# Kernel optimization log

Measured on AMD Instinct MI355X. Metric: run time of the kernel, lower is better.

The kernel has to match this reference:

```python
import jax, jax.numpy as jnp
import numpy as np

NUM_HEADS = 8

def _ln(x):
    m = x.mean(-1, keepdims=True)
    v = ((x - m) ** 2).mean(-1, keepdims=True)
    return (x - m) / jnp.sqrt(v + 1e-5)

def _encoder_layer(x, qkv_w, out_w, w1, w2, attn_mask=None):
    # standard post-LN transformer encoder layer; returns output and
    # head-averaged attention probabilities (b, t, t)
    b, t, d = x.shape
    dh = d // NUM_HEADS
    qkv = jnp.einsum('btd,cde->cbte', x, qkv_w)          # (3, b, t, d)
    q, k, v = [a.reshape(b, t, NUM_HEADS, dh).transpose(0, 2, 1, 3) for a in qkv]
    scores = jnp.einsum('bhqd,bhkd->bhqk', q, k) / jnp.sqrt(jnp.asarray(dh, x.dtype))
    if attn_mask is not None:
        scores = scores + attn_mask                       # additive -inf/0 mask
    probs = jax.nn.softmax(scores, axis=-1)
    ctx = jnp.einsum('bhqk,bhkd->bhqd', probs, v)
    ctx = ctx.transpose(0, 2, 1, 3).reshape(b, t, d)
    x = _ln(x + ctx @ out_w)
    x = _ln(x + jax.nn.relu(x @ w1) @ w2)
    return x, probs.mean(axis=1)

def _window_ids(wbool):
    # faithful vectorization of generate_local_window_mask_v2's sequential scan:
    # run-length segmentation of the thresholded weights, where a run of
    # length 1 is absorbed into the following run (weights[frame_start] is
    # overwritten). Returns per-frame window id (T,) int32.
    T = wbool.shape[0]
    def step(carry, t):
        cur, start, wid = carry
        wt = wbool[t]
        same = wt == cur
        merge = (~same) & (start + 1 == t)   # length-1 run absorbed
        close = (~same) & (~merge)           # close window, start new one
        cur = jnp.where(same, cur, wt)
        start = jnp.where(close, t, start)
        wid = wid + close.astype(jnp.int32)
        return (cur, start, wid), wid
    _, ids = jax.lax.scan(step, (wbool[0], jnp.int32(0), jnp.int32(0)), jnp.arange(1, T))
    return jnp.concatenate([jnp.zeros((1,), jnp.int32), ids])

def reference(x, v_qkv_w, v_out_w, v_w1, v_w2, l_qkv_w, l_out_w, l_w1, l_w2):
    b, t, d = x.shape
    # 1) vanilla transformer pass
    out_v, aw_v = _encoder_layer(x, v_qkv_w, v_out_w, v_w1, v_w2)
    # attention received per key token, min-max normalized (normalize_tensor)
    w = aw_v.sum(axis=1)                                   # (b, t)
    wmin = w.min(axis=-1, keepdims=True)
    wmax = w.max(axis=-1, keepdims=True)
    w = (w - wmin) / (wmax - wmin + 1e-8)
    # 2) dynamic window mask generation (threshold = 0.5)
    ids = jax.vmap(_window_ids)(w >= 0.5)                  # (b, t)
    same = ids[:, :, None] == ids[:, None, :]
    attn_mask = jnp.where(same, 0.0, -jnp.inf).astype(x.dtype)   # (b, t, t)
    # window_mapping[b, k, j] = 1 if frame j belongs to window k
    # (kept at full t rows; torch truncates to max_window_count, which is
    #  data-dependent; extra rows here are all-zero)
    window_mapping = (jnp.arange(t, dtype=jnp.int32)[None, :, None] == ids[:, None, :]).astype(x.dtype)
    # 3) dynamic-local-window transformer pass with block-diagonal mask
    out_l, aw_l = _encoder_layer(out_v, l_qkv_w, l_out_w, l_w1, l_w2,
                                 attn_mask=attn_mask[:, None])  # broadcast over heads
    aw_l = jnp.where(jnp.isneginf(aw_l), jnp.zeros_like(aw_l), aw_l)
    wl = jax.nn.softmax(aw_l.sum(axis=1), axis=-1)         # (b, t)
    # 4) window-weighted pooling
    word_tokens = jnp.einsum('bwt,btd->bwd', window_mapping, out_l * wl[:, :, None])
    return jnp.concatenate([word_tokens, x], axis=1), window_mapping

def setup_inputs() -> dict:
    B, T, D, FF = 8, 1024, 512, 2048
    key = jax.random.key(0)
    ks = jax.random.split(key, 9)
    s = 0.02
    return {
        'x': jax.random.normal(ks[0], (B, T, D), jnp.float32),
        'v_qkv_w': jax.random.normal(ks[1], (3, D, D), jnp.float32) * s,
        'v_out_w': jax.random.normal(ks[2], (D, D), jnp.float32) * s,
        'v_w1': jax.random.normal(ks[3], (D, FF), jnp.float32) * s,
        'v_w2': jax.random.normal(ks[4], (FF, D), jnp.float32) * s,
        'l_qkv_w': jax.random.normal(ks[5], (3, D, D), jnp.float32) * s,
        'l_out_w': jax.random.normal(ks[6], (D, D), jnp.float32) * s,
        'l_w1': jax.random.normal(ks[7], (D, FF), jnp.float32) * s,
        'l_w2': jax.random.normal(ks[8], (FF, D), jnp.float32) * s,
    }
```

## Files before the change

kernel.cpp:

```cpp
#include <hip/hip_runtime.h>
#include <math.h>

#define Bz 8
#define Tz 1024
#define Dz 512
#define FFz 2048
#define Hz 8
#define DHz 64
#define Mz (Bz * Tz)

typedef __attribute__((ext_vector_type(8))) short short8;
typedef __attribute__((ext_vector_type(4))) float f32x4;

__device__ inline unsigned short f2bf(float f) {
  unsigned u = __builtin_bit_cast(unsigned, f);
  return (unsigned short)((u + 0x7FFFu + ((u >> 16) & 1u)) >> 16);
}
__device__ inline float bf2f(unsigned short h) {
  unsigned u = (unsigned)h << 16;
  return __builtin_bit_cast(float, u);
}

__device__ inline void attn_decode(int g, int& b, int& h, int& qt) {
  const int xcd = g & 7;
  const int j = g >> 3;
  qt = j & 15;
  const int bh = ((j >> 4) << 3) | xcd;
  b = bh >> 3;
  h = bh & 7;
}

__device__ inline int swz(int row, int slotByte) {
  return row * 128 + (slotByte ^ ((row & 7) << 4));
}

struct WDesc { const float* src; unsigned short* dst; unsigned short* dstlo;
               int K; int N; int blk0; };
struct PrepArgs { WDesc d[12]; int nwc; };

__global__ __launch_bounds__(256) void prep_kernel(PrepArgs P,
    const float* __restrict__ x, unsigned short* __restrict__ xbf,
    unsigned short* __restrict__ xlo, float* __restrict__ csz)
{
  const int bid = blockIdx.x;
  const int tid = threadIdx.x;
  if (bid < P.nwc) {
    int i = 0;
    while (i < 11 && bid >= P.d[i + 1].blk0) ++i;
    const WDesc w = P.d[i];
    const int lb = bid - w.blk0;
    const int nbn = w.N / 32;
    const int bn = (lb % nbn) * 32, bk = (lb / nbn) * 32;
    __shared__ float t[32][33];
    const int tx = tid & 31, ty = tid >> 5;
#pragma unroll
    for (int r = 0; r < 32; r += 8)
      t[ty + r][tx] = w.src[(size_t)(bk + ty + r) * w.N + bn + tx];
    __syncthreads();
#pragma unroll
    for (int r = 0; r < 32; r += 8) {
      float v = t[tx][ty + r];
      unsigned short hv = f2bf(v);
      w.dst[(size_t)(bn + ty + r) * w.K + bk + tx] = hv;
      if (w.dstlo)
        w.dstlo[(size_t)(bn + ty + r) * w.K + bk + tx] = f2bf(v - bf2f(hv));
    }
  } else if (bid < P.nwc + 64) {
    int idx = (bid - P.nwc) * 256 + tid;
    csz[idx] = 0.f;
  } else {
    int i = (bid - P.nwc - 64) * 256 + tid;
    float4 v = *reinterpret_cast<const float4*>(&x[(size_t)i * 4]);
    ushort4 o, ol;
    o.x = f2bf(v.x); o.y = f2bf(v.y); o.z = f2bf(v.z); o.w = f2bf(v.w);
    ol.x = f2bf(v.x - bf2f(o.x)); ol.y = f2bf(v.y - bf2f(o.y));
    ol.z = f2bf(v.z - bf2f(o.z)); ol.w = f2bf(v.w - bf2f(o.w));
    *reinterpret_cast<ushort4*>(&xbf[(size_t)i * 4]) = o;
    *reinterpret_cast<ushort4*>(&xlo[(size_t)i * 4]) = ol;
  }
}

__global__ __launch_bounds__(256) void mfma_gemm_kernel(
    const unsigned short* __restrict__ A, const unsigned short* __restrict__ BT,
    void* __restrict__ p1, void* __restrict__ p2, void* __restrict__ p3,
    int K, int N, int mode)
{
  __shared__ unsigned short As[128 * 32];
  __shared__ unsigned short Bs[128 * 32];
  const int tid = threadIdx.x;
  const int lane = tid & 63, wave = tid >> 6;
  const int mr = lane & 15, quad = lane >> 4;
  const int wr = wave >> 1, wc = wave & 1;
  const int m0 = blockIdx.y * 128;
  const int n0 = blockIdx.x * 128;

  f32x4 acc[4][4];
  const f32x4 zero = {0.f, 0.f, 0.f, 0.f};
#pragma unroll
  for (int i = 0; i < 4; ++i)
#pragma unroll
    for (int j = 0; j < 4; ++j) acc[i][j] = zero;

  const int srow = tid >> 2;
  const int sslot = tid & 3;
  const unsigned short* Ag = A + (size_t)(m0 + srow) * K + sslot * 8;
  const unsigned short* Bg = BT + (size_t)(n0 + srow) * K + sslot * 8;
  char* AsB = (char*)As;
  char* BsB = (char*)Bs;

  for (int k0 = 0; k0 < K; k0 += 32) {
    short8 a0 = *reinterpret_cast<const short8*>(Ag + k0);
    short8 a1 = *reinterpret_cast<const short8*>(Ag + (size_t)64 * K + k0);
    short8 b0 = *reinterpret_cast<const short8*>(Bg + k0);
    short8 b1 = *reinterpret_cast<const short8*>(Bg + (size_t)64 * K + k0);
    *reinterpret_cast<short8*>(AsB + srow * 64 + sslot * 16) = a0;
    *reinterpret_cast<short8*>(AsB + (srow + 64) * 64 + sslot * 16) = a1;
    *reinterpret_cast<short8*>(BsB + srow * 64 + sslot * 16) = b0;
    *reinterpret_cast<short8*>(BsB + (srow + 64) * 64 + sslot * 16) = b1;
    __syncthreads();
    short8 af[4], bf[4];
#pragma unroll
    for (int i = 0; i < 4; ++i)
      af[i] = *reinterpret_cast<const short8*>(AsB + (wr * 64 + i * 16 + mr) * 64 + quad * 16);
#pragma unroll
    for (int j = 0; j < 4; ++j)
      bf[j] = *reinterpret_cast<const short8*>(BsB + (wc * 64 + j * 16 + mr) * 64 + quad * 16);
#pragma unroll
    for (int i = 0; i < 4; ++i)
#pragma unroll
      for (int j = 0; j < 4; ++j)
        acc[i][j] = __builtin_amdgcn_mfma_f32_16x16x32_bf16(af[i], bf[j], acc[i][j], 0, 0, 0);
    __syncthreads();
  }

  const int m0w = m0 + wr * 64;
  const int n0w = n0 + wc * 64;
  int emode = mode;
  unsigned short* Cbf = (unsigned short*)p1;
  unsigned short* Vt  = (unsigned short*)p1;
  int ncol = N, coff = 0;
  if (mode == 5) {
    if (n0w < 512)       { emode = 1; Cbf = (unsigned short*)p1; ncol = 512; coff = 0; }
    else if (n0w < 1024) { emode = 1; Cbf = (unsigned short*)p2; ncol = 512; coff = 512; }
    else                 { emode = 4; Vt = (unsigned short*)p3; coff = 1024; }
  }
  if (emode == 4) {
#pragma unroll
    for (int i = 0; i < 4; ++i)
#pragma unroll
      for (int j = 0; j < 4; ++j) {
        const int col = n0w - coff + j * 16 + mr;
        const int row0 = m0w + i * 16 + quad * 4;
        const int bb = row0 >> 10, t0 = row0 & 1023;
        ushort4 pk;
        pk.x = f2bf(acc[i][j][0]); pk.y = f2bf(acc[i][j][1]);
        pk.z = f2bf(acc[i][j][2]); pk.w = f2bf(acc[i][j][3]);
        *reinterpret_cast<ushort4*>(
            &Vt[((size_t)((bb * Hz + (col >> 6)) * DHz + (col & 63))) * Tz + t0]) = pk;
      }
  } else if (emode == 0) {
    float* Cf = (float*)p1;
#pragma unroll
    for (int i = 0; i < 4; ++i)
#pragma unroll
      for (int j = 0; j < 4; ++j) {
        const int col = n0w + j * 16 + mr;
#pragma unroll
        for (int rr = 0; rr < 4; ++rr)
          Cf[(size_t)(m0w + i * 16 + quad * 4 + rr) * N + col] = acc[i][j][rr];
      }
  } else {
    const bool relu = (emode == 2);
#pragma unroll
    for (int i = 0; i < 4; ++i)
#pragma unroll
      for (int j = 0; j < 4; ++j) {
        const int col = n0w - coff + j * 16 + mr;
#pragma unroll
        for (int rr = 0; rr < 4; ++rr) {
          float v = acc[i][j][rr];
          if (relu) v = fmaxf(v, 0.f);
          Cbf[(size_t)(m0w + i * 16 + quad * 4 + rr) * ncol + col] = f2bf(v);
        }
      }
  }
}

__global__ __launch_bounds__(256) void gemm_qk_mfma_kernel(
    const unsigned short* __restrict__ Xh, const unsigned short* __restrict__ Xl,
    const unsigned short* __restrict__ WQh, const unsigned short* __restrict__ WQl,
    const unsigned short* __restrict__ WKh, const unsigned short* __restrict__ WKl,
    unsigned short* __restrict__ Qhi, unsigned short* __restrict__ Qlo,
    unsigned short* __restrict__ Khi, unsigned short* __restrict__ Klo)
{
  __shared__ unsigned short Ash[128 * 32];
  __shared__ unsigned short Asl[128 * 32];
  __shared__ unsigned short Bsh[128 * 32];
  __shared__ unsigned short Bsl[128 * 32];
  const int tid = threadIdx.x;
  const int lane = tid & 63, wave = tid >> 6;
  const int mr = lane & 15, quad = lane >> 4;
  const int wr = wave >> 1, wc = wave & 1;
  const int sel = blockIdx.y >> 6;
  const int m0 = (blockIdx.y & 63) * 128;
  const int n0 = blockIdx.x * 128;
  const unsigned short* Bh = sel ? WKh : WQh;
  const unsigned short* Bl = sel ? WKl : WQl;
  unsigned short* Chi = sel ? Khi : Qhi;
  unsigned short* Clo = sel ? Klo : Qlo;

  f32x4 acc[4][4];
  const f32x4 zero = {0.f, 0.f, 0.f, 0.f};
#pragma unroll
  for (int i = 0; i < 4; ++i)
#pragma unroll
    for (int j = 0; j < 4; ++j) acc[i][j] = zero;

  const int srow = tid >> 2;
  const int sslot = tid & 3;
  const unsigned short* Ahg = Xh + (size_t)(m0 + srow) * Dz + sslot * 8;
  const unsigned short* Alg = Xl + (size_t)(m0 + srow) * Dz + sslot * 8;
  const unsigned short* Bhg = Bh + (size_t)(n0 + srow) * Dz + sslot * 8;
  const unsigned short* Blg = Bl + (size_t)(n0 + srow) * Dz + sslot * 8;
  char* AhB = (char*)Ash; char* AlB = (char*)Asl;
  char* BhB = (char*)Bsh; char* BlB = (char*)Bsl;

  for (int k0 = 0; k0 < Dz; k0 += 32) {
    short8 ah0 = *reinterpret_cast<const short8*>(Ahg + k0);
    short8 ah1 = *reinterpret_cast<const short8*>(Ahg + (size_t)64 * Dz + k0);
    short8 al0 = *reinterpret_cast<const short8*>(Alg + k0);
    short8 al1 = *reinterpret_cast<const short8*>(Alg + (size_t)64 * Dz + k0);
    short8 bh0 = *reinterpret_cast<const short8*>(Bhg + k0);
    short8 bh1 = *reinterpret_cast<const short8*>(Bhg + (size_t)64 * Dz + k0);
    short8 bl0 = *reinterpret_cast<const short8*>(Blg + k0);
    short8 bl1 = *reinterpret_cast<const short8*>(Blg + (size_t)64 * Dz + k0);
    *reinterpret_cast<short8*>(AhB + srow * 64 + sslot * 16) = ah0;
    *reinterpret_cast<short8*>(AhB + (srow + 64) * 64 + sslot * 16) = ah1;
    *reinterpret_cast<short8*>(AlB + srow * 64 + sslot * 16) = al0;
    *reinterpret_cast<short8*>(AlB + (srow + 64) * 64 + sslot * 16) = al1;
    *reinterpret_cast<short8*>(BhB + srow * 64 + sslot * 16) = bh0;
    *reinterpret_cast<short8*>(BhB + (srow + 64) * 64 + sslot * 16) = bh1;
    *reinterpret_cast<short8*>(BlB + srow * 64 + sslot * 16) = bl0;
    *reinterpret_cast<short8*>(BlB + (srow + 64) * 64 + sslot * 16) = bl1;
    __syncthreads();
    short8 ah[4], al[4], bh[4], bl[4];
#pragma unroll
    for (int i = 0; i < 4; ++i) {
      const int ab = (wr * 64 + i * 16 + mr) * 64 + quad * 16;
      ah[i] = *reinterpret_cast<const short8*>(AhB + ab);
      al[i] = *reinterpret_cast<const short8*>(AlB + ab);
    }
#pragma unroll
    for (int j = 0; j < 4; ++j) {
      const int bb = (wc * 64 + j * 16 + mr) * 64 + quad * 16;
      bh[j] = *reinterpret_cast<const short8*>(BhB + bb);
      bl[j] = *reinterpret_cast<const short8*>(BlB + bb);
    }
#pragma unroll
    for (int i = 0; i < 4; ++i)
#pragma unroll
      for (int j = 0; j < 4; ++j) {
        acc[i][j] = __builtin_amdgcn_mfma_f32_16x16x32_bf16(al[i], bh[j], acc[i][j], 0, 0, 0);
        acc[i][j] = __builtin_amdgcn_mfma_f32_16x16x32_bf16(ah[i], bl[j], acc[i][j], 0, 0, 0);
        acc[i][j] = __builtin_amdgcn_mfma_f32_16x16x32_bf16(ah[i], bh[j], acc[i][j], 0, 0, 0);
      }
    __syncthreads();
  }

  const int m0w = m0 + wr * 64;
  const int n0w = n0 + wc * 64;
#pragma unroll
  for (int i = 0; i < 4; ++i)
#pragma unroll
    for (int j = 0; j < 4; ++j) {
      const int col = n0w + j * 16 + mr;
#pragma unroll
      for (int rr = 0; rr < 4; ++rr) {
        const size_t row = (size_t)(m0w + i * 16 + quad * 4 + rr);
        float v = acc[i][j][rr];
        unsigned short hv = f2bf(v);
        Chi[row * Dz + col] = hv;
        Clo[row * Dz + col] = f2bf(v - bf2f(hv));
      }
    }
}

__global__ __launch_bounds__(256) void attn_z_kernel(
    const unsigned short* __restrict__ Qh, const unsigned short* __restrict__ Kh,
    float* __restrict__ invzG)
{
  __shared__ unsigned short Ksh[64 * 64];
  const int tid = threadIdx.x;
  const int lane = tid & 63, wave = tid >> 6;
  const int c = lane & 15, quad = lane >> 4;
  int b, h, qt;
  attn_decode(blockIdx.x, b, h, qt);
  const size_t bT = (size_t)b * Tz;
  const int qrow = qt * 64 + wave * 16;
  const int hoff = h * DHz;

  const size_t qbase = (bT + qrow + c) * Dz + hoff + quad * 8;
  short8 q0 = *reinterpret_cast<const short8*>(Qh + qbase);
  short8 q1 = *reinterpret_cast<const short8*>(Qh + qbase + 32);

  const int sr = tid >> 3;
  const int sj = (tid & 7) * 16;
  const unsigned short* khb = Kh + (bT + sr) * Dz + hoff + (tid & 7) * 8;
  char* KshB = (char*)Ksh;

  const f32x4 zf = {0.f, 0.f, 0.f, 0.f};
  float z[4] = {0.f, 0.f, 0.f, 0.f};

  for (int t = 0; t < 16; ++t) {
    const int k0 = t * 64;
    short8 g0 = *reinterpret_cast<const short8*>(khb + (size_t)k0 * Dz);
    short8 g1 = *reinterpret_cast<const short8*>(khb + (size_t)(k0 + 32) * Dz);
    *reinterpret_cast<short8*>(KshB + swz(sr, sj)) = g0;
    *reinterpret_cast<short8*>(KshB + swz(sr + 32, sj)) = g1;
    __syncthreads();
#pragma unroll
    for (int sub = 0; sub < 4; ++sub) {
      const int row = sub * 16 + c;
      short8 kh0 = *reinterpret_cast<const short8*>(KshB + swz(row, quad * 16));
      short8 kh1 = *reinterpret_cast<const short8*>(KshB + swz(row, 64 + quad * 16));
      f32x4 aA = zf, aB = zf;
      aA = __builtin_amdgcn_mfma_f32_16x16x32_bf16(q0, kh0, aA, 0, 0, 0);
      aB = __builtin_amdgcn_mfma_f32_16x16x32_bf16(q1, kh1, aB, 0, 0, 0);
#pragma unroll
      for (int rr = 0; rr < 4; ++rr) z[rr] += __expf((aA[rr] + aB[rr]) * 0.125f);
    }
    __syncthreads();
  }
#pragma unroll
  for (int w = 1; w < 16; w <<= 1) {
#pragma unroll
    for (int rr = 0; rr < 4; ++rr) z[rr] += __shfl_xor(z[rr], w);
  }
  if (c == 0) {
#pragma unroll
    for (int rr = 0; rr < 4; ++rr)
      invzG[(size_t)(b * Hz + h) * Tz + qrow + quad * 4 + rr] = 1.f / z[rr];
  }
}

__global__ __launch_bounds__(256) void attn_ctx_kernel(
    const unsigned short* __restrict__ Qh, const unsigned short* __restrict__ Ql,
    const unsigned short* __restrict__ Kh, const unsigned short* __restrict__ Kl,
    const unsigned short* __restrict__ Vt, const float* __restrict__ invzG,
    unsigned short* __restrict__ ctx, float* __restrict__ part)
{
  __shared__ unsigned short Ksh[64 * 64];
  __shared__ unsigned short Ksl[64 * 64];
  __shared__ unsigned short Vsh[64 * 64];
  __shared__ unsigned short Pld[64][76];
  __shared__ float CSPt[4][64];
  const int tid = threadIdx.x;
  const int lane = tid & 63, wave = tid >> 6;
  const int c = lane & 15, quad = lane >> 4;
  int b, h, qt;
  attn_decode(blockIdx.x, b, h, qt);
  const size_t bT = (size_t)b * Tz;
  const int qrow = qt * 64 + wave * 16;
  const int hoff = h * DHz;
  const int lidx = b * 128 + h * 16 + qt;

  const size_t qbase = (bT + qrow + c) * Dz + hoff + quad * 8;
  short8 q0h = *reinterpret_cast<const short8*>(Qh + qbase);
  short8 q1h = *reinterpret_cast<const short8*>(Qh + qbase + 32);
  short8 q0l = *reinterpret_cast<const short8*>(Ql + qbase);
  short8 q1l = *reinterpret_cast<const short8*>(Ql + qbase + 32);

  float invz[4];
#pragma unroll
  for (int rr = 0; rr < 4; ++rr)
    invz[rr] = invzG[(size_t)(b * Hz + h) * Tz + qrow + quad * 4 + rr];

  const int sr = tid >> 3;
  const int sj = (tid & 7) * 16;
  const unsigned short* khb = Kh + (bT + sr) * Dz + hoff + (tid & 7) * 8;
  const unsigned short* klb = Kl + (bT + sr) * Dz + hoff + (tid & 7) * 8;
  const unsigned short* vtb = Vt + ((size_t)(b * Hz + h) * DHz + sr) * Tz + (tid & 7) * 8;

  const f32x4 zf = {0.f, 0.f, 0.f, 0.f};
  f32x4 ot[4] = {zf, zf, zf, zf};

  char* KshB = (char*)Ksh;
  char* KslB = (char*)Ksl;
  char* VshB = (char*)Vsh;

  for (int t = 0; t < 16; ++t) {
    const int k0 = t * 64;
    short8 g0 = *reinterpret_cast<const short8*>(khb + (size_t)k0 * Dz);
    short8 g1 = *reinterpret_cast<const short8*>(khb + (size_t)(k0 + 32) * Dz);
    short8 g2 = *reinterpret_cast<const short8*>(klb + (size_t)k0 * Dz);
    short8 g3 = *reinterpret_cast<const short8*>(klb + (size_t)(k0 + 32) * Dz);
    short8 g4 = *reinterpret_cast<const short8*>(vtb + k0);
    short8 g5 = *reinterpret_cast<const short8*>(vtb + 32 * Tz + k0);
    *reinterpret_cast<short8*>(KshB + swz(sr, sj)) = g0;
    *reinterpret_cast<short8*>(KshB + swz(sr + 32, sj)) = g1;
    *reinterpret_cast<short8*>(KslB + swz(sr, sj)) = g2;
    *reinterpret_cast<short8*>(KslB + swz(sr + 32, sj)) = g3;
    *reinterpret_cast<short8*>(VshB + swz(sr, sj)) = g4;
    *reinterpret_cast<short8*>(VshB + swz(sr + 32, sj)) = g5;
    __syncthreads();

#pragma unroll
    for (int sub = 0; sub < 4; ++sub) {
      const int row = sub * 16 + c;
      short8 kh0 = *reinterpret_cast<const short8*>(KshB + swz(row, quad * 16));
      short8 kh1 = *reinterpret_cast<const short8*>(KshB + swz(row, 64 + quad * 16));
      short8 kl0 = *reinterpret_cast<const short8*>(KslB + swz(row, quad * 16));
      short8 kl1 = *reinterpret_cast<const short8*>(KslB + swz(row, 64 + quad * 16));
      f32x4 aA = zf, aB = zf;
      aA = __builtin_amdgcn_mfma_f32_16x16x32_bf16(q0h, kh0, aA, 0, 0, 0);
      aB = __builtin_amdgcn_mfma_f32_16x16x32_bf16(q1h, kh1, aB, 0, 0, 0);
      aA = __builtin_amdgcn_mfma_f32_16x16x32_bf16(q0h, kl0, aA, 0, 0, 0);
      aB = __builtin_amdgcn_mfma_f32_16x16x32_bf16(q1h, kl1, aB, 0, 0, 0);
      aA = __builtin_amdgcn_mfma_f32_16x16x32_bf16(q0l, kh0, aA, 0, 0, 0);
      aB = __builtin_amdgcn_mfma_f32_16x16x32_bf16(q1l, kh1, aB, 0, 0, 0);
      float p[4];
#pragma unroll
      for (int rr = 0; rr < 4; ++rr)
        p[rr] = __expf((aA[rr] + aB[rr]) * 0.125f) * invz[rr];
      float cs = p[0] + p[1] + p[2] + p[3];
      cs += __shfl_xor(cs, 16);
      cs += __shfl_xor(cs, 32);
      if (quad == 0) CSPt[wave][sub * 16 + c] = cs;
#pragma unroll
      for (int rr = 0; rr < 4; ++rr)
        Pld[(wave << 4) + quad * 4 + rr][sub * 16 + c] = f2bf(p[rr]);
    }

    union { short8 v; ushort4 hh[2]; } pb0, pb1;
    pb0.hh[0] = *reinterpret_cast<const ushort4*>(&Pld[(wave << 4) + c][quad * 8]);
    pb0.hh[1] = *reinterpret_cast<const ushort4*>(&Pld[(wave << 4) + c][quad * 8 + 4]);
    pb1.hh[0] = *reinterpret_cast<const ushort4*>(&Pld[(wave << 4) + c][32 + quad * 8]);
    pb1.hh[1] = *reinterpret_cast<const ushort4*>(&Pld[(wave << 4) + c][32 + quad * 8 + 4]);
#pragma unroll
    for (int ds = 0; ds < 4; ++ds) {
      const int row = ds * 16 + c;
      short8 v0 = *reinterpret_cast<const short8*>(VshB + swz(row, quad * 16));
      short8 v1 = *reinterpret_cast<const short8*>(VshB + swz(row, 64 + quad * 16));
      ot[ds] = __builtin_amdgcn_mfma_f32_16x16x32_bf16(v0, pb0.v, ot[ds], 0, 0, 0);
      ot[ds] = __builtin_amdgcn_mfma_f32_16x16x32_bf16(v1, pb1.v, ot[ds], 0, 0, 0);
    }
    __syncthreads();

    if (tid < 64) {
      float v = ((CSPt[0][tid] + CSPt[1][tid]) + CSPt[2][tid]) + CSPt[3][tid];
      part[(size_t)lidx * 1024 + k0 + tid] = v * (1.f / Hz);
    }
  }

  const size_t cb = (bT + qrow + c) * Dz + hoff;
#pragma unroll
  for (int ds = 0; ds < 4; ++ds) {
    ushort4 pk;
    pk.x = f2bf(ot[ds][0]); pk.y = f2bf(ot[ds][1]);
    pk.z = f2bf(ot[ds][2]); pk.w = f2bf(ot[ds][3]);
    *reinterpret_cast<ushort4*>(&ctx[cb + ds * 16 + quad * 4]) = pk;
  }
}

__global__ __launch_bounds__(256) void colsum_reduce_kernel(
    const float* __restrict__ part, float* __restrict__ colsum)
{
  const int i = blockIdx.x * 256 + threadIdx.x;
  const int b = i >> 10, k = i & 1023;
  const float* p = part + (size_t)(b * 128) * 1024 + k;
  float s = 0.f;
  for (int j = 0; j < 128; ++j) s += p[(size_t)j * 1024];
  colsum[i] = s;
}

__global__ __launch_bounds__(256) void attn_mfma2_kernel(
    const unsigned short* __restrict__ Qh, const unsigned short* __restrict__ Kh,
    const unsigned short* __restrict__ Vt, const int* __restrict__ ids,
    const int* __restrict__ wst,
    unsigned short* __restrict__ ctx, float* __restrict__ colsum)
{
  __shared__ unsigned short Pld[64][76];
  __shared__ float csb[1024];

  const int tid = threadIdx.x;
  const int lane = tid & 63, wave = tid >> 6;
  const int c = lane & 15, quad = lane >> 4;
  int b, h, qt;
  attn_decode(blockIdx.x, b, h, qt);
  const size_t bT = (size_t)b * Tz;
  const int qrow = qt * 64 + wave * 16;
  const int hoff = h * DHz;

  for (int i = tid; i < 1024; i += 256) csb[i] = 0.f;

  const int id_lo = ids[bT + qt * 64];
  const int id_hi = ids[bT + qt * 64 + 63];
  const int klo = wst[b * (Tz + 1) + id_lo];
  const int khi = wst[b * (Tz + 1) + id_hi + 1];
  const int t0 = klo >> 6, t1 = (khi - 1) >> 6;

  const size_t qbase = (bT + qrow + c) * Dz + hoff + quad * 8;
  short8 q0 = *reinterpret_cast<const short8*>(Qh + qbase);
  short8 q1 = *reinterpret_cast<const short8*>(Qh + qbase + 32);

  int qid[4];
#pragma unroll
  for (int rr = 0; rr < 4; ++rr) qid[rr] = ids[bT + qrow + quad * 4 + rr];
  __syncthreads();

  const f32x4 zf = {0.f, 0.f, 0.f, 0.f};

  float z[4] = {0.f, 0.f, 0.f, 0.f};
  for (int t = t0; t <= t1; ++t) {
    const int k0 = t * 64;
#pragma unroll
    for (int sub = 0; sub < 4; ++sub) {
      const size_t kb = (bT + k0 + sub * 16 + c) * Dz + hoff + quad * 8;
      short8 kh0 = *reinterpret_cast<const short8*>(Kh + kb);
      short8 kh1 = *reinterpret_cast<const short8*>(Kh + kb + 32);
      f32x4 acc = zf;
      acc = __builtin_amdgcn_mfma_f32_16x16x32_bf16(q0, kh0, acc, 0, 0, 0);
      acc = __builtin_amdgcn_mfma_f32_16x16x32_bf16(q1, kh1, acc, 0, 0, 0);
      int kidv = ids[bT + k0 + sub * 16 + c];
#pragma unroll
      for (int rr = 0; rr < 4; ++rr) {
        float e = __expf(acc[rr] * 0.125f);
        if (qid[rr] != kidv) e = 0.f;
        z[rr] += e;
      }
    }
  }
#pragma unroll
  for (int w = 1; w < 16; w <<= 1) {
#pragma unroll
    for (int rr = 0; rr < 4; ++rr) z[rr] += __shfl_xor(z[rr], w);
  }
  float invz[4];
#pragma unroll
  for (int rr = 0; rr < 4; ++rr) invz[rr] = 1.f / z[rr];

  f32x4 ot[4] = {zf, zf, zf, zf};
  for (int t = t0; t <= t1; ++t) {
    const int k0 = t * 64;
#pragma unroll
    for (int sub = 0; sub < 4; ++sub) {
      const size_t kb = (bT + k0 + sub * 16 + c) * Dz + hoff + quad * 8;
      short8 kh0 = *reinterpret_cast<const short8*>(Kh + kb);
      short8 kh1 = *reinterpret_cast<const short8*>(Kh + kb + 32);
      f32x4 acc = zf;
      acc = __builtin_amdgcn_mfma_f32_16x16x32_bf16(q0, kh0, acc, 0, 0, 0);
      acc = __builtin_amdgcn_mfma_f32_16x16x32_bf16(q1, kh1, acc, 0, 0, 0);
      int kidv = ids[bT + k0 + sub * 16 + c];
      float p[4];
#pragma unroll
      for (int rr = 0; rr < 4; ++rr) {
        float e = __expf(acc[rr] * 0.125f);
        if (qid[rr] != kidv) e = 0.f;
        p[rr] = e * invz[rr];
      }
      float cs = p[0] + p[1] + p[2] + p[3];
      cs += __shfl_xor(cs, 16);
      cs += __shfl_xor(cs, 32);
      if (quad == 0) atomicAdd(&csb[k0 + sub * 16 + c], cs);
#pragma unroll
      for (int rr = 0; rr < 4; ++rr)
        Pld[(wave << 4) + quad * 4 + rr][sub * 16 + c] = f2bf(p[rr]);
    }
    union { short8 v; ushort4 hh[2]; } pb0, pb1;
    pb0.hh[0] = *reinterpret_cast<const ushort4*>(&Pld[(wave << 4) + c][quad * 8]);
    pb0.hh[1] = *reinterpret_cast<const ushort4*>(&Pld[(wave << 4) + c][quad * 8 + 4]);
    pb1.hh[0] = *reinterpret_cast<const ushort4*>(&Pld[(wave << 4) + c][32 + quad * 8]);
    pb1.hh[1] = *reinterpret_cast<const ushort4*>(&Pld[(wave << 4) + c][32 + quad * 8 + 4]);
#pragma unroll
    for (int ds = 0; ds < 4; ++ds) {
      const size_t va = ((size_t)((b * Hz + h) * DHz + ds * 16 + c)) * Tz + k0 + quad * 8;
      short8 v0 = *reinterpret_cast<const short8*>(Vt + va);
      short8 v1 = *reinterpret_cast<const short8*>(Vt + va + 32);
      ot[ds] = __builtin_amdgcn_mfma_f32_16x16x32_bf16(v0, pb0.v, ot[ds], 0, 0, 0);
      ot[ds] = __builtin_amdgcn_mfma_f32_16x16x32_bf16(v1, pb1.v, ot[ds], 0, 0, 0);
    }
  }

  const size_t cb = (bT + qrow + c) * Dz + hoff;
#pragma unroll
  for (int ds = 0; ds < 4; ++ds) {
    ushort4 pk;
    pk.x = f2bf(ot[ds][0]); pk.y = f2bf(ot[ds][1]);
    pk.z = f2bf(ot[ds][2]); pk.w = f2bf(ot[ds][3]);
    *reinterpret_cast<ushort4*>(&ctx[cb + ds * 16 + quad * 4]) = pk;
  }
  __syncthreads();
  for (int i = tid; i < 1024; i += 256)
    atomicAdd(&colsum[bT + i], csb[i] * (1.f / Hz));
}

__global__ __launch_bounds__(256) void ln_kernel(const float* __restrict__ residf,
    const unsigned short* __restrict__ residbf, const float* __restrict__ delta,
    float* __restrict__ outf, unsigned short* __restrict__ outbf)
{
  const size_t base = (size_t)blockIdx.x * Dz;
  const int tid = threadIdx.x;
  float r0, r1;
  if (residf) {
    r0 = residf[base + tid]; r1 = residf[base + tid + 256];
  } else {
    r0 = bf2f(residbf[base + tid]); r1 = bf2f(residbf[base + tid + 256]);
  }
  float x0 = r0 + delta[base + tid];
  float x1 = r1 + delta[base + tid + 256];
  __shared__ float red[4];
  float s = x0 + x1;
#pragma unroll
  for (int off = 32; off; off >>= 1) s += __shfl_down(s, off);
  if ((tid & 63) == 0) red[tid >> 6] = s;
  __syncthreads();
  const float mean = (red[0] + red[1] + red[2] + red[3]) * (1.f / Dz);
  __syncthreads();
  float d0 = x0 - mean, d1 = x1 - mean;
  float v = d0 * d0 + d1 * d1;
#pragma unroll
  for (int off = 32; off; off >>= 1) v += __shfl_down(v, off);
  if ((tid & 63) == 0) red[tid >> 6] = v;
  __syncthreads();
  const float var = (red[0] + red[1] + red[2] + red[3]) * (1.f / Dz);
  const float rstd = rsqrtf(var + 1e-5f);
  float y0 = d0 * rstd, y1 = d1 * rstd;
  if (outf) {
    outf[base + tid] = y0;
    outf[base + tid + 256] = y1;
  }
  outbf[base + tid] = f2bf(y0);
  outbf[base + tid + 256] = f2bf(y1);
}

__global__ __launch_bounds__(256) void window_ids_kernel(const float* __restrict__ cs,
    int* __restrict__ ids, int* __restrict__ wst, int* __restrict__ nwin)
{
  const int b = blockIdx.x, tid = threadIdx.x;
  __shared__ float vals[Tz];
  __shared__ int swst[Tz + 1];
  __shared__ unsigned long long words[16];
  __shared__ float rmin[4], rmax[4];
  __shared__ int snw;
  float mn = INFINITY, mx = -INFINITY;
  for (int t = tid; t < Tz; t += 256) {
    float v = cs[b * Tz + t];
    vals[t] = v;
    mn = fminf(mn, v); mx = fmaxf(mx, v);
  }
#pragma unroll
  for (int off = 32; off; off >>= 1) {
    mn = fminf(mn, __shfl_down(mn, off));
    mx = fmaxf(mx, __shfl_down(mx, off));
  }
  if ((tid & 63) == 0) { rmin[tid >> 6] = mn; rmax[tid >> 6] = mx; }
  __syncthreads();
  mn = fminf(fminf(rmin[0], rmin[1]), fminf(rmin[2], rmin[3]));
  mx = fmaxf(fmaxf(rmax[0], rmax[1]), fmaxf(rmax[2], rmax[3]));
  const float inv = 1.f / (mx - mn + 1e-8f);
  const int lane = tid & 63, wave = tid >> 6;
#pragma unroll
  for (int pass = 0; pass < 4; ++pass) {
    const int t = pass * 256 + wave * 64 + lane;
    const bool bit = ((vals[t] - mn) * inv) >= 0.5f;
    unsigned long long m = __ballot(bit);
    if (lane == 0) words[pass * 4 + wave] = m;
  }
  __syncthreads();
  if (tid == 0) {
    int start = 0, wid = 0;
    swst[0] = 0;
    unsigned long long carry = 0;
    for (int i = 0; i < 16; ++i) {
      const unsigned long long wi = words[i];
      unsigned long long tr = wi ^ ((wi << 1) | carry);
      carry = wi >> 63;
      if (i == 0) tr &= ~1ULL;
      while (tr) {
        const int t = i * 64 + __builtin_ctzll(tr);
        tr &= tr - 1;
        if (start + 1 != t) { start = t; ++wid; swst[wid] = t; }
      }
    }
    nwin[b] = wid + 1;
    swst[wid + 1] = Tz;
    snw = wid + 1;
  }
  __syncthreads();
  const int nw = snw;
  for (int j = tid; j <= nw; j += 256) wst[b * (Tz + 1) + j] = swst[j];
  for (int t = tid; t < Tz; t += 256) {
    int lo = 0, hi = nw;
    while (hi - lo > 1) {
      const int mid = (lo + hi) >> 1;
      if (swst[mid] <= t) lo = mid; else hi = mid;
    }
    ids[b * Tz + t] = lo;
  }
}

__global__ __launch_bounds__(256) void wl_softmax_kernel(const float* __restrict__ cs,
                                                         float* __restrict__ wl)
{
  const int b = blockIdx.x, tid = threadIdx.x;
  __shared__ float vals[Tz];
  __shared__ float red[4];
  float mx = -INFINITY;
  for (int t = tid; t < Tz; t += 256) {
    float v = cs[b * Tz + t];
    vals[t] = v;
    mx = fmaxf(mx, v);
  }
#pragma unroll
  for (int off = 32; off; off >>= 1) mx = fmaxf(mx, __shfl_down(mx, off));
  if ((tid & 63) == 0) red[tid >> 6] = mx;
  __syncthreads();
  mx = fmaxf(fmaxf(red[0], red[1]), fmaxf(red[2], red[3]));
  __syncthreads();
  float se = 0.f;
  for (int t = tid; t < Tz; t += 256) {
    float e = expf(vals[t] - mx);
    vals[t] = e;
    se += e;
  }
#pragma unroll
  for (int off = 32; off; off >>= 1) se += __shfl_down(se, off);
  if ((tid & 63) == 0) red[tid >> 6] = se;
  __syncthreads();
  const float inv = 1.f / (red[0] + red[1] + red[2] + red[3]);
  for (int t = tid; t < Tz; t += 256) wl[b * Tz + t] = vals[t] * inv;
}

__global__ __launch_bounds__(256) void outputs_kernel(
    const unsigned short* __restrict__ outl, const float* __restrict__ wl,
    const int* __restrict__ wst, const int* __restrict__ nwin,
    const int* __restrict__ ids, const float* __restrict__ x,
    float* __restrict__ out, float* __restrict__ out2)
{
  const int bid = blockIdx.x;
  const int tid = threadIdx.x;
  if (bid < 8192) {
    const int w = bid & (Tz - 1);
    const int b = bid >> 10;
    float a0 = 0.f, a1 = 0.f;
    if (w < nwin[b]) {
      const int s = wst[b * (Tz + 1) + w], e = wst[b * (Tz + 1) + w + 1];
      for (int t = s; t < e; ++t) {
        const float sc = wl[b * Tz + t];
        const unsigned short* p = &outl[((size_t)(b * Tz + t)) * Dz];
        a0 += bf2f(p[tid]) * sc;
        a1 += bf2f(p[tid + 256]) * sc;
      }
    }
    float* o = &out[((size_t)(b * 2 * Tz + w)) * Dz];
    o[tid] = a0;
    o[tid + 256] = a1;
  } else if (bid < 16384) {
    const int lb = bid - 8192;
    const int w = lb & (Tz - 1);
    const int b = lb >> 10;
    const int j = tid * 4;
    int4 id4 = *reinterpret_cast<const int4*>(&ids[b * Tz + j]);
    float4 v;
    v.x = (id4.x == w) ? 1.f : 0.f;
    v.y = (id4.y == w) ? 1.f : 0.f;
    v.z = (id4.z == w) ? 1.f : 0.f;
    v.w = (id4.w == w) ? 1.f : 0.f;
    *reinterpret_cast<float4*>(&out2[((size_t)(b * Tz + w)) * Tz + j]) = v;
  } else {
    size_t i = (size_t)(bid - 16384) * 256 + tid;
    size_t idx = i * 4;
    size_t rowi = idx >> 9;
    size_t d = idx & 511;
    size_t b = rowi >> 10, t = rowi & 1023;
    float4 v = *reinterpret_cast<const float4*>(&x[idx]);
    *reinterpret_cast<float4*>(&out[(((b * 2 * Tz) + Tz + t) << 9) + d]) = v;
  }
}

extern "C" void kernel_launch(void* const* d_in, const int* in_sizes, int n_in,
                              void* d_out, int out_size, void* d_ws, size_t ws_size,
                              hipStream_t stream)
{
  (void)in_sizes; (void)n_in; (void)out_size; (void)ws_size;
  const float* x     = (const float*)d_in[0];
  const float* vqkv  = (const float*)d_in[1];
  const float* voutw = (const float*)d_in[2];
  const float* vw1   = (const float*)d_in[3];
  const float* vw2   = (const float*)d_in[4];
  const float* lqkv  = (const float*)d_in[5];
  const float* loutw = (const float*)d_in[6];
  const float* lw1   = (const float*)d_in[7];
  const float* lw2   = (const float*)d_in[8];
  float* out = (float*)d_out;
  float* ws  = (float*)d_ws;

  unsigned short* QLbf = (unsigned short*)(ws + 0);
  unsigned short* KLbf = (unsigned short*)(ws + 2097152);
  float* PROJ = ws + 0;
  float* Y1   = ws + 4194304;
  unsigned short* QHbf = (unsigned short*)(ws + 8388608);
  unsigned short* KHbf = (unsigned short*)(ws + 10485760);
  unsigned short* VT   = (unsigned short*)(ws + 12582912);
  unsigned short* SLOT1 = (unsigned short*)(ws + 14680064);
  unsigned short* SLOT2 = (unsigned short*)(ws + 16777216);
  unsigned short* HIDbf = (unsigned short*)(ws + 18874368);
  unsigned short* XBF   = (unsigned short*)(ws + 18874368);
  float* PART = ws + 18874368;
  unsigned short* XLO = (unsigned short*)(ws + 20971520);
  unsigned short* WVQV = (unsigned short*)(ws + 27262976);
  unsigned short* WVO  = (unsigned short*)(ws + 27394048);
  unsigned short* WV1  = (unsigned short*)(ws + 27525120);
  unsigned short* WV2  = (unsigned short*)(ws + 28049408);
  unsigned short* WLQ0 = (unsigned short*)(ws + 28573696);
  unsigned short* WLQ1 = (unsigned short*)(ws + 28704768);
  unsigned short* WLQ2 = (unsigned short*)(ws + 28835840);
  unsigned short* WLO  = (unsigned short*)(ws + 28966912);
  unsigned short* WL1  = (unsigned short*)(ws + 29097984);
  unsigned short* WL2  = (unsigned short*)(ws + 29622272);
  float* CS1   = ws + 30146560;
  float* CS2   = ws + 30154752;
  float* WLs   = ws + 30162944;
  int*   IDS   = (int*)(ws + 30171136);
  int*   WST   = (int*)(ws + 30179328);
  int*   NWIN  = (int*)(ws + 30187776);
  float* INVZ  = ws + 30195968;
  unsigned short* WQH = (unsigned short*)(ws + 30261504);
  unsigned short* WQL = (unsigned short*)(ws + 30392576);
  unsigned short* WKH = (unsigned short*)(ws + 30523648);
  unsigned short* WKL = (unsigned short*)(ws + 30654720);

  dim3 blk(256);

  PrepArgs P;
  auto setw = [&](int i, const float* s, unsigned short* d, unsigned short* dl,
                  int K, int N, int b0) {
    P.d[i].src = s; P.d[i].dst = d; P.d[i].dstlo = dl;
    P.d[i].K = K; P.d[i].N = N; P.d[i].blk0 = b0;
  };
  int b0 = 0;
  setw(0, vqkv + 2 * Dz * Dz, WVQV, nullptr, Dz, Dz, b0); b0 += 256;
  setw(1, voutw, WVO, nullptr, Dz, Dz, b0); b0 += 256;
  setw(2, vw1, WV1, nullptr, Dz, FFz, b0); b0 += 1024;
  setw(3, vw2, WV2, nullptr, FFz, Dz, b0); b0 += 1024;
  setw(4, lqkv + 0 * Dz * Dz, WLQ0, nullptr, Dz, Dz, b0); b0 += 256;
  setw(5, lqkv + 1 * Dz * Dz, WLQ1, nullptr, Dz, Dz, b0); b0 += 256;
  setw(6, lqkv + 2 * Dz * Dz, WLQ2, nullptr, Dz, Dz, b0); b0 += 256;
  setw(7, loutw, WLO, nullptr, Dz, Dz, b0); b0 += 256;
  setw(8, lw1, WL1, nullptr, Dz, FFz, b0); b0 += 1024;
  setw(9, lw2, WL2, nullptr, FFz, Dz, b0); b0 += 1024;
  setw(10, vqkv + 0 * Dz * Dz, WQH, WQL, Dz, Dz, b0); b0 += 256;
  setw(11, vqkv + 1 * Dz * Dz, WKH, WKL, Dz, Dz, b0); b0 += 256;
  P.nwc = b0;
  prep_kernel<<<dim3(P.nwc + 64 + 4096), blk, 0, stream>>>(P, x, XBF, XLO, CS1);

  auto mgemm = [&](const unsigned short* A, const unsigned short* BT, void* p1,
                   void* p2, void* p3, int K, int N, int mode) {
    mfma_gemm_kernel<<<dim3(N / 128, Mz / 128), dim3(256), 0, stream>>>(
        A, BT, p1, p2, p3, K, N, mode);
  };

  gemm_qk_mfma_kernel<<<dim3(4, 128), dim3(256), 0, stream>>>(
      XBF, XLO, WQH, WQL, WKH, WKL, QHbf, QLbf, KHbf, KLbf);
  attn_z_kernel<<<dim3(Bz * Hz * 16), blk, 0, stream>>>(QHbf, KHbf, INVZ);
  mgemm(XBF, WVQV, VT, nullptr, nullptr, Dz, Dz, 4);
  attn_ctx_kernel<<<dim3(Bz * Hz * 16), blk, 0, stream>>>(
      QHbf, QLbf, KHbf, KLbf, VT, INVZ, SLOT1, PART);
  colsum_reduce_kernel<<<dim3(32), blk, 0, stream>>>(PART, CS1);
  window_ids_kernel<<<dim3(Bz), blk, 0, stream>>>(CS1, IDS, WST, NWIN);
  mgemm(SLOT1, WVO, PROJ, nullptr, nullptr, Dz, Dz, 0);
  ln_kernel<<<dim3(Mz), blk, 0, stream>>>(x, nullptr, PROJ, Y1, SLOT2);
  mgemm(SLOT2, WV1, HIDbf, nullptr, nullptr, Dz, FFz, 2);
  mgemm(HIDbf, WV2, PROJ, nullptr, nullptr, FFz, Dz, 0);
  ln_kernel<<<dim3(Mz), blk, 0, stream>>>(Y1, nullptr, PROJ, nullptr, SLOT2);

  mgemm(SLOT2, WLQ0, QHbf, KHbf, VT, Dz, 3 * Dz, 5);
  attn_mfma2_kernel<<<dim3(Bz * Hz * 16), blk, 0, stream>>>(
      QHbf, KHbf, VT, IDS, WST, SLOT1, CS2);
  mgemm(SLOT1, WLO, PROJ, nullptr, nullptr, Dz, Dz, 0);
  ln_kernel<<<dim3(Mz), blk, 0, stream>>>(nullptr, SLOT2, PROJ, Y1, SLOT2);
  mgemm(SLOT2, WL1, HIDbf, nullptr, nullptr, Dz, FFz, 2);
  mgemm(HIDbf, WL2, PROJ, nullptr, nullptr, FFz, Dz, 0);
  ln_kernel<<<dim3(Mz), blk, 0, stream>>>(Y1, nullptr, PROJ, nullptr, SLOT2);

  wl_softmax_kernel<<<dim3(Bz), blk, 0, stream>>>(CS2, WLs);
  outputs_kernel<<<dim3(20480), blk, 0, stream>>>(SLOT2, WLs, WST, NWIN, IDS, x,
                                                  out, out + (size_t)Bz * 2 * Tz * Dz);
}
```

Measured before the change: 599.5 us.

## Use direct global-to-LDS loads in GEMMs and stage K/V tiles in LDS for attention

The two GEMM kernels now fill their shared-memory tiles with global_load_lds, so data goes straight to LDS instead of passing through registers. Each wave loads its own 16-row slice. The windowed attention kernel now stages each 64-key K tile and V^T tile cooperatively into swizzled LDS, so the four waves no longer each read the same K/V rows from global memory. This cuts redundant global traffic and register pressure, at the cost of extra block-wide barriers per key tile and more shared memory per block.

```diff
diff --git a/kernel.cpp b/kernel.cpp
--- a/kernel.cpp
+++ b/kernel.cpp
@@ -19,6 +19,12 @@
 __device__ inline float bf2f(unsigned short h) {
   unsigned u = (unsigned)h << 16;
   return __builtin_bit_cast(float, u);
+}
+
+__device__ inline void gll16(const unsigned short* g, unsigned short* l) {
+  __builtin_amdgcn_global_load_lds(
+      (const __attribute__((address_space(1))) void*)g,
+      (__attribute__((address_space(3))) void*)l, 16, 0, 0);
 }
 
 __device__ inline void attn_decode(int g, int& b, int& h, int& qt) {
@@ -101,22 +107,23 @@
 #pragma unroll
     for (int j = 0; j < 4; ++j) acc[i][j] = zero;
 
-  const int srow = tid >> 2;
-  const int sslot = tid & 3;
-  const unsigned short* Ag = A + (size_t)(m0 + srow) * K + sslot * 8;
-  const unsigned short* Bg = BT + (size_t)(n0 + srow) * K + sslot * 8;
+  const int lrow = lane >> 2, lslot = lane & 3;
+  const unsigned short* Ag0 = A + (size_t)(m0 + wave * 16 + lrow) * K + lslot * 8;
+  const unsigned short* Ag1 = A + (size_t)(m0 + 64 + wave * 16 + lrow) * K + lslot * 8;
+  const unsigned short* Bg0 = BT + (size_t)(n0 + wave * 16 + lrow) * K + lslot * 8;
+  const unsigned short* Bg1 = BT + (size_t)(n0 + 64 + wave * 16 + lrow) * K + lslot * 8;
+  unsigned short* Al0 = As + wave * 512;
+  unsigned short* Al1 = As + 2048 + wave * 512;
+  unsigned short* Bl0 = Bs + wave * 512;
+  unsigned short* Bl1 = Bs + 2048 + wave * 512;
   char* AsB = (char*)As;
   char* BsB = (char*)Bs;
 
   for (int k0 = 0; k0 < K; k0 += 32) {
-    short8 a0 = *reinterpret_cast<const short8*>(Ag + k0);
-    short8 a1 = *reinterpret_cast<const short8*>(Ag + (size_t)64 * K + k0);
-    short8 b0 = *reinterpret_cast<const short8*>(Bg + k0);
-    short8 b1 = *reinterpret_cast<const short8*>(Bg + (size_t)64 * K + k0);
-    *reinterpret_cast<short8*>(AsB + srow * 64 + sslot * 16) = a0;
-    *reinterpret_cast<short8*>(AsB + (srow + 64) * 64 + sslot * 16) = a1;
-    *reinterpret_cast<short8*>(BsB + srow * 64 + sslot * 16) = b0;
-    *reinterpret_cast<short8*>(BsB + (srow + 64) * 64 + sslot * 16) = b1;
+    gll16(Ag0 + k0, Al0);
+    gll16(Ag1 + k0, Al1);
+    gll16(Bg0 + k0, Bl0);
+    gll16(Bg1 + k0, Bl1);
     __syncthreads();
     short8 af[4], bf[4];
 #pragma unroll
@@ -216,32 +223,27 @@
 #pragma unroll
     for (int j = 0; j < 4; ++j) acc[i][j] = zero;
 
-  const int srow = tid >> 2;
-  const int sslot = tid & 3;
-  const unsigned short* Ahg = Xh + (size_t)(m0 + srow) * Dz + sslot * 8;
-  const unsigned short* Alg = Xl + (size_t)(m0 + srow) * Dz + sslot * 8;
-  const unsigned short* Bhg = Bh + (size_t)(n0 + srow) * Dz + sslot * 8;
-  const unsigned short* Blg = Bl + (size_t)(n0 + srow) * Dz + sslot * 8;
+  const int lrow = lane >> 2, lslot = lane & 3;
+  const unsigned short* gAh0 = Xh + (size_t)(m0 + wave * 16 + lrow) * Dz + lslot * 8;
+  const unsigned short* gAh1 = Xh + (size_t)(m0 + 64 + wave * 16 + lrow) * Dz + lslot * 8;
+  const unsigned short* gAl0 = Xl + (size_t)(m0 + wave * 16 + lrow) * Dz + lslot * 8;
+  const unsigned short* gAl1 = Xl + (size_t)(m0 + 64 + wave * 16 + lrow) * Dz + lslot * 8;
+  const unsigned short* gBh0 = Bh + (size_t)(n0 + wave * 16 + lrow) * Dz + lslot * 8;
+  const unsigned short* gBh1 = Bh + (size_t)(n0 + 64 + wave * 16 + lrow) * Dz + lslot * 8;
+  const unsigned short* gBl0 = Bl + (size_t)(n0 + wave * 16 + lrow) * Dz + lslot * 8;
+  const unsigned short* gBl1 = Bl + (size_t)(n0 + 64 + wave * 16 + lrow) * Dz + lslot * 8;
+  unsigned short* LAh0 = Ash + wave * 512; unsigned short* LAh1 = Ash + 2048 + wave * 512;
+  unsigned short* LAl0 = Asl + wave * 512; unsigned short* LAl1 = Asl + 2048 + wave * 512;
+  unsigned short* LBh0 = Bsh + wave * 512; unsigned short* LBh1 = Bsh + 2048 + wave * 512;
+  unsigned short* LBl0 = Bsl + wave * 512; unsigned short* LBl1 = Bsl + 2048 + wave * 512;
   char* AhB = (char*)Ash; char* AlB = (char*)Asl;
   char* BhB = (char*)Bsh; char* BlB = (char*)Bsl;
 
   for (int k0 = 0; k0 < Dz; k0 += 32) {
-    short8 ah0 = *reinterpret_cast<const short8*>(Ahg + k0);
-    short8 ah1 = *reinterpret_cast<const short8*>(Ahg + (size_t)64 * Dz + k0);
-    short8 al0 = *reinterpret_cast<const short8*>(Alg + k0);
-    short8 al1 = *reinterpret_cast<const short8*>(Alg + (size_t)64 * Dz + k0);
-    short8 bh0 = *reinterpret_cast<const short8*>(Bhg + k0);
-    short8 bh1 = *reinterpret_cast<const short8*>(Bhg + (size_t)64 * Dz + k0);
-    short8 bl0 = *reinterpret_cast<const short8*>(Blg + k0);
-    short8 bl1 = *reinterpret_cast<const short8*>(Blg + (size_t)64 * Dz + k0);
-    *reinterpret_cast<short8*>(AhB + srow * 64 + sslot * 16) = ah0;
-    *reinterpret_cast<short8*>(AhB + (srow + 64) * 64 + sslot * 16) = ah1;
-    *reinterpret_cast<short8*>(AlB + srow * 64 + sslot * 16) = al0;
-    *reinterpret_cast<short8*>(AlB + (srow + 64) * 64 + sslot * 16) = al1;
-    *reinterpret_cast<short8*>(BhB + srow * 64 + sslot * 16) = bh0;
-    *reinterpret_cast<short8*>(BhB + (srow + 64) * 64 + sslot * 16) = bh1;
-    *reinterpret_cast<short8*>(BlB + srow * 64 + sslot * 16) = bl0;
-    *reinterpret_cast<short8*>(BlB + (srow + 64) * 64 + sslot * 16) = bl1;
+    gll16(gAh0 + k0, LAh0); gll16(gAh1 + k0, LAh1);
+    gll16(gAl0 + k0, LAl0); gll16(gAl1 + k0, LAl1);
+    gll16(gBh0 + k0, LBh0); gll16(gBh1 + k0, LBh1);
+    gll16(gBl0 + k0, LBl0); gll16(gBl1 + k0, LBl1);
     __syncthreads();
     short8 ah[4], al[4], bh[4], bl[4];
 #pragma unroll
@@ -479,6 +481,8 @@
     const int* __restrict__ wst,
     unsigned short* __restrict__ ctx, float* __restrict__ colsum)
 {
+  __shared__ unsigned short Ksh[64 * 64];
+  __shared__ unsigned short Vsh[64 * 64];
   __shared__ unsigned short Pld[64][76];
   __shared__ float csb[1024];
 
@@ -506,6 +510,13 @@
   int qid[4];
 #pragma unroll
   for (int rr = 0; rr < 4; ++rr) qid[rr] = ids[bT + qrow + quad * 4 + rr];
+
+  const int sr = tid >> 3;
+  const int sj = (tid & 7) * 16;
+  const unsigned short* khb = Kh + (bT + sr) * Dz + hoff + (tid & 7) * 8;
+  const unsigned short* vtb = Vt + ((size_t)(b * Hz + h) * DHz + sr) * Tz + (tid & 7) * 8;
+  char* KshB = (char*)Ksh;
+  char* VshB = (char*)Vsh;
   __syncthreads();
 
   const f32x4 zf = {0.f, 0.f, 0.f, 0.f};
@@ -513,11 +524,16 @@
   float z[4] = {0.f, 0.f, 0.f, 0.f};
   for (int t = t0; t <= t1; ++t) {
     const int k0 = t * 64;
+    short8 g0 = *reinterpret_cast<const short8*>(khb + (size_t)k0 * Dz);
+    short8 g1 = *reinterpret_cast<const short8*>(khb + (size_t)(k0 + 32) * Dz);
+    *reinterpret_cast<short8*>(KshB + swz(sr, sj)) = g0;
+    *reinterpret_cast<short8*>(KshB + swz(sr + 32, sj)) = g1;
+    __syncthreads();
 #pragma unroll
     for (int sub = 0; sub < 4; ++sub) {
-      const size_t kb = (bT + k0 + sub * 16 + c) * Dz + hoff + quad * 8;
-      short8 kh0 = *reinterpret_cast<const short8*>(Kh + kb);
-      short8 kh1 = *reinterpret_cast<const short8*>(Kh + kb + 32);
+      const int row = sub * 16 + c;
+      short8 kh0 = *reinterpret_cast<const short8*>(KshB + swz(row, quad * 16));
+      short8 kh1 = *reinterpret_cast<const short8*>(KshB + swz(row, 64 + quad * 16));
       f32x4 acc = zf;
       acc = __builtin_amdgcn_mfma_f32_16x16x32_bf16(q0, kh0, acc, 0, 0, 0);
       acc = __builtin_amdgcn_mfma_f32_16x16x32_bf16(q1, kh1, acc, 0, 0, 0);
@@ -529,6 +545,7 @@
         z[rr] += e;
       }
     }
+    __syncthreads();
   }
 #pragma unroll
   for (int w = 1; w < 16; w <<= 1) {
@@ -542,11 +559,20 @@
   f32x4 ot[4] = {zf, zf, zf, zf};
   for (int t = t0; t <= t1; ++t) {
     const int k0 = t * 64;
+    short8 g0 = *reinterpret_cast<const short8*>(khb + (size_t)k0 * Dz);
+    short8 g1 = *reinterpret_cast<const short8*>(khb + (size_t)(k0 + 32) * Dz);
+    short8 g4 = *reinterpret_cast<const short8*>(vtb + k0);
+    short8 g5 = *reinterpret_cast<const short8*>(vtb + 32 * Tz + k0);
+    *reinterpret_cast<short8*>(KshB + swz(sr, sj)) = g0;
+    *reinterpret_cast<short8*>(KshB + swz(sr + 32, sj)) = g1;
+    *reinterpret_cast<short8*>(VshB + swz(sr, sj)) = g4;
+    *reinterpret_cast<short8*>(VshB + swz(sr + 32, sj)) = g5;
+    __syncthreads();
 #pragma unroll
     for (int sub = 0; sub < 4; ++sub) {
-      const size_t kb = (bT + k0 + sub * 16 + c) * Dz + hoff + quad * 8;
-      short8 kh0 = *reinterpret_cast<const short8*>(Kh + kb);
-      short8 kh1 = *reinterpret_cast<const short8*>(Kh + kb + 32);
+      const int row = sub * 16 + c;
+      short8 kh0 = *reinterpret_cast<const short8*>(KshB + swz(row, quad * 16));
+      short8 kh1 = *reinterpret_cast<const short8*>(KshB + swz(row, 64 + quad * 16));
       f32x4 acc = zf;
       acc = __builtin_amdgcn_mfma_f32_16x16x32_bf16(q0, kh0, acc, 0, 0, 0);
       acc = __builtin_amdgcn_mfma_f32_16x16x32_bf16(q1, kh1, acc, 0, 0, 0);
@@ -573,12 +599,13 @@
     pb1.hh[1] = *reinterpret_cast<const ushort4*>(&Pld[(wave << 4) + c][32 + quad * 8 + 4]);
 #pragma unroll
     for (int ds = 0; ds < 4; ++ds) {
-      const size_t va = ((size_t)((b * Hz + h) * DHz + ds * 16 + c)) * Tz + k0 + quad * 8;
-      short8 v0 = *reinterpret_cast<const short8*>(Vt + va);
-      short8 v1 = *reinterpret_cast<const short8*>(Vt + va + 32);
+      const int row = ds * 16 + c;
+      short8 v0 = *reinterpret_cast<const short8*>(VshB + swz(row, quad * 16));
+      short8 v1 = *reinterpret_cast<const short8*>(VshB + swz(row, 64 + quad * 16));
       ot[ds] = __builtin_amdgcn_mfma_f32_16x16x32_bf16(v0, pb0.v, ot[ds], 0, 0, 0);
       ot[ds] = __builtin_amdgcn_mfma_f32_16x16x32_bf16(v1, pb1.v, ot[ds], 0, 0, 0);
     }
+    __syncthreads();
   }
 
   const size_t cb = (bT + qrow + c) * Dz + hoff;
```

Measured after the change: 582.5 us. -2.8%, faster.
